# Kernel tuning notes

Hardware: AMD Instinct MI355X
Metric: run time of the kernel (lower is better)

The kernel has to match this reference:

```python
import jax, jax.numpy as jnp
from jax import lax
import numpy as np

# ---- static config (matches init_kwargs) ----
B, H, W = 8, 32, 32
L = H * W                      # 1024 tokens
D_MODEL = 384
MAMBA_DIM = 192                # d_model * d_mamba_ratio
LOCAL_DIM = 192
D_INNER = 384                  # expand_m * MAMBA_DIM
D_STATE = 16
D_CONV = 4
DT_RANK = 12                   # ceil(MAMBA_DIM / 16)
NDIR = 4                       # h, h_flip, v, v_flip
RED = 48                       # int(D_INNER * 0.125), BiAttn reduce dim
INNER_C = 192                  # LOCAL_DIM * expand_c
K_C = 8                        # local block depthwise kernel size


def setup_inputs() -> dict:
    key = jax.random.key(0)
    ks = jax.random.split(key, 16)
    s = 0.02
    return {
        "x": jax.random.normal(ks[0], (B, L, D_MODEL), jnp.float32),
        "in_proj_w": jax.random.normal(ks[1], (2 * D_INNER, MAMBA_DIM)) * s,
        "A_log": jnp.broadcast_to(jnp.log(jnp.arange(1, D_STATE + 1, dtype=jnp.float32)), (NDIR, D_INNER, D_STATE)) + 0.0,
        "conv_w": jax.random.normal(ks[2], (NDIR, D_INNER, D_CONV)) * 0.2,
        "conv_b": jax.random.normal(ks[3], (NDIR, D_INNER)) * 0.02,
        "xproj_w": jax.random.normal(ks[4], (NDIR, DT_RANK + 2 * D_STATE, D_INNER)) * s,
        "dtproj_w": jax.random.normal(ks[5], (NDIR, D_INNER, DT_RANK)) * (DT_RANK ** -0.5),
        "dtproj_b": jax.random.normal(ks[6], (NDIR, D_INNER)) * 0.5 - 4.0,
        "Dp": jnp.ones((NDIR, D_INNER)),
        "out_proj_w": jax.random.normal(ks[7], (MAMBA_DIM, D_INNER)) * s,
        "attn_ln_g": jnp.ones((D_INNER,)),
        "attn_ln_b": jnp.zeros((D_INNER,)),
        "attn_gr_w": jax.random.normal(ks[8], (RED, D_INNER)) * s,
        "attn_gr_b": jnp.zeros((RED,)),
        "attn_cs_w": jax.random.normal(ks[9], (D_INNER, RED)) * s,
        "attn_cs_b": jnp.zeros((D_INNER,)),
        "pw1_w": jax.random.normal(ks[10], (2 * INNER_C, LOCAL_DIM)) * s,
        "pw1_b": jnp.zeros((2 * INNER_C,)),
        "dw_w": jax.random.normal(ks[11], (INNER_C, K_C)) * 0.2,
        "dw_b": jnp.zeros((INNER_C,)),
        "bn_g": jnp.ones((INNER_C,)),
        "bn_b": jnp.zeros((INNER_C,)),
        "pw2_w": jax.random.normal(ks[12], (LOCAL_DIM, INNER_C)) * s,
        "pw2_b": jnp.zeros((LOCAL_DIM,)),
    }


def _forward(x, in_proj_w, A_log, conv_w, conv_b, xproj_w, dtproj_w, dtproj_b, Dp,
             out_proj_w, attn_ln_g, attn_ln_b, attn_gr_w, attn_gr_b, attn_cs_w, attn_cs_b,
             pw1_w, pw1_b, dw_w, dw_b, bn_g, bn_b, pw2_w, pw2_b):
    mamba_in = x[:, :, :MAMBA_DIM]
    local_in = x[:, :, MAMBA_DIM:]

    # ---------- MultiMamba branch ----------
    xz = jnp.swapaxes(mamba_in @ in_proj_w.T, 1, 2)   # (B, 2*D_INNER, L)

    def to_dir(t, i):
        # reorder channel-last-token axis per scan direction
        if i == 0:
            return t
        if i == 1:
            return jnp.flip(t, -1)
        tv = t.reshape(B, -1, H, W).swapaxes(-1, -2).reshape(B, -1, L)  # column-major scan
        return tv if i == 2 else jnp.flip(tv, -1)

    def from_dir(t, i):
        if i == 0:
            return t
        if i == 1:
            return jnp.flip(t, -1)
        if i == 3:
            t = jnp.flip(t, -1)
        return t.reshape(B, -1, W, H).swapaxes(-1, -2).reshape(B, -1, L)

    def ssm_dir(xzd, i):
        # mamba_inner_fn_no_out_proj: causal dwconv -> silu -> x_proj -> selective scan -> gate
        xp, z = jnp.split(xzd, 2, axis=1)            # (B, D_INNER, L) each
        xpad = jnp.pad(xp, ((0, 0), (0, 0), (D_CONV - 1, 0)))
        u = lax.conv_general_dilated(xpad, conv_w[i][:, None, :], (1,), 'VALID',
                                     dimension_numbers=('NCH', 'OIH', 'NCH'),
                                     feature_group_count=D_INNER)
        u = jax.nn.silu(u + conv_b[i][None, :, None])
        dbl = jnp.einsum('bdl,rd->brl', u, xproj_w[i])
        dt = dbl[:, :DT_RANK]
        Bm = dbl[:, DT_RANK:DT_RANK + D_STATE]
        Cm = dbl[:, DT_RANK + D_STATE:]
        delta = jax.nn.softplus(jnp.einsum('brl,dr->bdl', dt, dtproj_w[i]) + dtproj_b[i][None, :, None])
        A = -jnp.exp(A_log[i])                        # (D_INNER, D_STATE)

        def step(h, inps):
            d_t, B_t, C_t, u_t = inps                 # (B,d),(B,n),(B,n),(B,d)
            h = jnp.exp(d_t[:, :, None] * A) * h + (d_t * u_t)[:, :, None] * B_t[:, None, :]
            return h, jnp.einsum('bdn,bn->bd', h, C_t)

        h0 = jnp.zeros((B, D_INNER, D_STATE), x.dtype)
        _, ys = lax.scan(step, h0, (delta.transpose(2, 0, 1), Bm.transpose(2, 0, 1),
                                    Cm.transpose(2, 0, 1), u.transpose(2, 0, 1)))
        y = ys.transpose(1, 2, 0) + u * Dp[i][:, None]  # (B, D_INNER, L)
        return y * jax.nn.silu(z)

    def biattn(t):                                     # (B, L, D_INNER)
        mu = t.mean(-1, keepdims=True)
        var = ((t - mu) ** 2).mean(-1, keepdims=True)
        tn = (t - mu) / jnp.sqrt(var + 1e-5) * attn_ln_g + attn_ln_b
        g = tn.mean(1, keepdims=True)                  # global pool (B,1,D_INNER)
        g = jax.nn.gelu(g @ attn_gr_w.T + attn_gr_b, approximate=False)
        c = jax.nn.sigmoid(g @ attn_cs_w.T + attn_cs_b)
        return t * c

    acc = jnp.zeros((B, L, D_INNER), x.dtype)
    for i in range(NDIR):                              # fixed small set of directions
        out_i = from_dir(ssm_dir(to_dir(xz, i), i), i)
        acc = acc + biattn(jnp.swapaxes(out_i, 1, 2))
    mamba_out = acc @ out_proj_w.T                     # (B, L, MAMBA_DIM)

    # ---------- Local conv branch ----------
    hch = jnp.einsum('blc,oc->bol', local_in, pw1_w) + pw1_b[None, :, None]
    a, gte = jnp.split(hch, 2, axis=1)
    hch = a * jax.nn.sigmoid(gte)                      # GLU, (B, INNER_C, L)
    pad_l = K_C // 2
    pad_r = K_C // 2 - (K_C + 1) % 2                   # calc_same_padding(8) -> (4, 3)
    hpad = jnp.pad(hch, ((0, 0), (0, 0), (pad_l, pad_r)))
    hch = lax.conv_general_dilated(hpad, dw_w[:, None, :], (1,), 'VALID',
                                   dimension_numbers=('NCH', 'OIH', 'NCH'),
                                   feature_group_count=INNER_C) + dw_b[None, :, None]
    mu = hch.mean((0, 2))                              # BatchNorm1d (training-mode batch stats)
    var = hch.var((0, 2))
    hch = (hch - mu[None, :, None]) / jnp.sqrt(var + 1e-5)[None, :, None] * bn_g[None, :, None] + bn_b[None, :, None]
    hch = hch * jax.nn.sigmoid(hch)                    # Swish
    local_out = jnp.einsum('bcl,oc->blo', hch, pw2_w) + pw2_b

    return jnp.concatenate([mamba_out, local_out], axis=-1)


def reference(x, in_proj_w, A_log, conv_w, conv_b, xproj_w, dtproj_w, dtproj_b, Dp,
              out_proj_w, attn_ln_g, attn_ln_b, attn_gr_w, attn_gr_b, attn_cs_w, attn_cs_b,
              pw1_w, pw1_b, dw_w, dw_b, bn_g, bn_b, pw2_w, pw2_b):
    return _forward(x, in_proj_w, A_log, conv_w, conv_b, xproj_w, dtproj_w, dtproj_b, Dp,
                    out_proj_w, attn_ln_g, attn_ln_b, attn_gr_w, attn_gr_b, attn_cs_w, attn_cs_b,
                    pw1_w, pw1_b, dw_w, dw_b, bn_g, bn_b, pw2_w, pw2_b)
```

## Files before the change

kernel.cpp:

```cpp
#include <hip/hip_runtime.h>
#include <stdint.h>


#define DEV __device__ __forceinline__

typedef __attribute__((ext_vector_type(8))) short short8;
typedef __attribute__((ext_vector_type(4))) short short4v;
typedef __attribute__((ext_vector_type(4))) float f32x4;

DEV float bf(ushort v) { union { uint32_t u; float f; } c; c.u = ((uint32_t)v) << 16; return c.f; }
DEV ushort fbf(float f) {
  union { float f; uint32_t u; } c; c.f = f;
  uint32_t u = c.u;
  return (ushort)((u + 0x7FFFu + ((u >> 16) & 1u)) >> 16);
}

#if __has_builtin(__builtin_amdgcn_exp2f)
DEV float fexp2(float x) { return __builtin_amdgcn_exp2f(x); }
#else
DEV float fexp2(float x) { return __expf(x * 0.6931471805599453f); }
#endif

template<int CTRL>
DEV float rradd(float x) {
  return x + __int_as_float(__builtin_amdgcn_update_dpp(
      0, __float_as_int(x), CTRL, 0xF, 0xF, true));
}

DEV int pmap(int i, int j) {
  if (i == 0) return j;
  if (i == 1) return 1023 - j;
  if (i == 2) return ((j & 31) << 5) | (j >> 5);
  int k = 1023 - j; return ((k & 31) << 5) | (k >> 5);
}

DEV void cvt4(const float* __restrict__ s, ushort* __restrict__ d, int blk, int tid) {
  const int idx = (blk * 256 + tid) * 4;
  float4 v = *(const float4*)(s + idx);
  d[idx] = fbf(v.x); d[idx + 1] = fbf(v.y); d[idx + 2] = fbf(v.z); d[idx + 3] = fbf(v.w);
}

__global__ __launch_bounds__(256) void prep_all(
    const float* __restrict__ x, ushort* __restrict__ xb,
    const float* __restrict__ ipw, ushort* __restrict__ ipwb,
    const float* __restrict__ opw, ushort* __restrict__ opwb,
    const float* __restrict__ pw1w, ushort* __restrict__ pw1wb,
    const float* __restrict__ pw2w, ushort* __restrict__ pw2wb,
    const float* __restrict__ xw, ushort* __restrict__ xwp)
{
  const int bx = blockIdx.x, tid = threadIdx.x;
  if (bx < 3072)      cvt4(x, xb, bx, tid);
  else if (bx < 3216) cvt4(ipw, ipwb, bx - 3072, tid);
  else if (bx < 3288) cvt4(opw, opwb, bx - 3216, tid);
  else if (bx < 3360) cvt4(pw1w, pw1wb, bx - 3288, tid);
  else if (bx < 3396) cvt4(pw2w, pw2wb, bx - 3360, tid);
  else {
    const int row = bx - 3396;
    const int i = row >> 6, nn = row & 63;
    for (int c = tid; c < 384; c += 256)
      xwp[(size_t)row * 384 + c] = (nn < 44) ? fbf(xw[((size_t)i * 44 + nn) * 384 + c]) : (ushort)0;
  }
}

template<bool BF16OUT, bool BIAS>
__global__ __launch_bounds__(256) void gemm_bt(
    const ushort* __restrict__ A, long long sAz, int lda,
    const ushort* __restrict__ Bw, long long sBz,
    const float* __restrict__ bias,
    void* __restrict__ C, long long sCz, int ldc, int coff, int K)
{
  __shared__ ushort As[64][40];
  __shared__ ushort Bs[64][40];
  A += (size_t)blockIdx.z * sAz;
  Bw += (size_t)blockIdx.z * sBz;
  const int tid = threadIdx.x;
  const int m0 = blockIdx.x * 64, n0 = blockIdx.y * 64;
  const int w = tid >> 6, lane = tid & 63, l15 = lane & 15, quad = lane >> 4;
  const int sr = tid >> 2, sc = (tid & 3) * 8;
  f32x4 acc[4] = {};
  for (int k0 = 0; k0 < K; k0 += 32) {
    __syncthreads();
    *(short8*)&As[sr][sc] = *(const short8*)(A + (size_t)(m0 + sr) * lda + k0 + sc);
    *(short8*)&Bs[sr][sc] = *(const short8*)(Bw + (size_t)(n0 + sr) * K + k0 + sc);
    __syncthreads();
    short8 av = *(short8*)&As[w * 16 + l15][quad * 8];
#pragma unroll
    for (int nt = 0; nt < 4; nt++) {
      short8 bv = *(short8*)&Bs[nt * 16 + l15][quad * 8];
      acc[nt] = __builtin_amdgcn_mfma_f32_16x16x32_bf16(av, bv, acc[nt], 0, 0, 0);
    }
  }
  float* cf = (float*)C + (size_t)blockIdx.z * sCz;
  ushort* cb = (ushort*)C + (size_t)blockIdx.z * sCz;
#pragma unroll
  for (int nt = 0; nt < 4; nt++) {
    const int col = n0 + nt * 16 + l15;
    const float bv = BIAS ? bias[col] : 0.f;
#pragma unroll
    for (int r = 0; r < 4; r++) {
      const int row = m0 + w * 16 + quad * 4 + r;
      float v = acc[nt][r] + bv;
      if (BF16OUT) cb[(size_t)row * ldc + coff + col] = fbf(v);
      else         cf[(size_t)row * ldc + coff + col] = v;
    }
  }
}

__global__ __launch_bounds__(256) void gemm_dual(
    const ushort* __restrict__ A0, int lda0, const ushort* __restrict__ B0,
    const float* __restrict__ bias0, void* __restrict__ C0, int ldc0, int coff0, int K0,
    int nt0, int bf0,
    const ushort* __restrict__ A1, int lda1, const ushort* __restrict__ B1,
    const float* __restrict__ bias1, void* __restrict__ C1, int ldc1, int coff1, int K1,
    int bf1, float* __restrict__ bnsum)
{
  __shared__ ushort As[64][40];
  __shared__ ushort Bs[64][40];
  if (blockIdx.x == 0 && blockIdx.y == 0) {
    for (int k = threadIdx.x; k < 384; k += 256) bnsum[k] = 0.f;
  }
  const ushort* A; const ushort* Bw; const float* bias; void* C;
  int lda, ldc, coff, K, bf16o, n0;
  if ((int)blockIdx.y < nt0) {
    A = A0; lda = lda0; Bw = B0; bias = bias0; C = C0; ldc = ldc0; coff = coff0; K = K0;
    bf16o = bf0; n0 = blockIdx.y * 64;
  } else {
    A = A1; lda = lda1; Bw = B1; bias = bias1; C = C1; ldc = ldc1; coff = coff1; K = K1;
    bf16o = bf1; n0 = (blockIdx.y - nt0) * 64;
  }
  const int tid = threadIdx.x;
  const int m0 = blockIdx.x * 64;
  const int w = tid >> 6, lane = tid & 63, l15 = lane & 15, quad = lane >> 4;
  const int sr = tid >> 2, sc = (tid & 3) * 8;
  f32x4 acc[4] = {};
  for (int k0 = 0; k0 < K; k0 += 32) {
    __syncthreads();
    *(short8*)&As[sr][sc] = *(const short8*)(A + (size_t)(m0 + sr) * lda + k0 + sc);
    *(short8*)&Bs[sr][sc] = *(const short8*)(Bw + (size_t)(n0 + sr) * K + k0 + sc);
    __syncthreads();
    short8 av = *(short8*)&As[w * 16 + l15][quad * 8];
#pragma unroll
    for (int nt = 0; nt < 4; nt++) {
      short8 bv = *(short8*)&Bs[nt * 16 + l15][quad * 8];
      acc[nt] = __builtin_amdgcn_mfma_f32_16x16x32_bf16(av, bv, acc[nt], 0, 0, 0);
    }
  }
#pragma unroll
  for (int nt = 0; nt < 4; nt++) {
    const int col = n0 + nt * 16 + l15;
    const float bv = bias ? bias[col] : 0.f;
#pragma unroll
    for (int r = 0; r < 4; r++) {
      const int row = m0 + w * 16 + quad * 4 + r;
      float v = acc[nt][r] + bv;
      if (bf16o) ((ushort*)C)[(size_t)row * ldc + coff + col] = fbf(v);
      else       ((float*)C)[(size_t)row * ldc + coff + col] = v;
    }
  }
}

__global__ __launch_bounds__(256) void gemm_pw2(
    const float* __restrict__ h2, const float* __restrict__ bnsum,
    const float* __restrict__ bng, const float* __restrict__ bnb,
    const ushort* __restrict__ Bw, const float* __restrict__ bias,
    float* __restrict__ C)
{
  __shared__ ushort As[64][40];
  __shared__ ushort Bs[64][40];
  __shared__ float bsc[192], bsh[192];
  const int tid = threadIdx.x;
  const int m0 = blockIdx.x * 64, n0 = blockIdx.y * 64;
  const int w = tid >> 6, lane = tid & 63, l15 = lane & 15, quad = lane >> 4;
  const int sr = tid >> 2, sc = (tid & 3) * 8;
  for (int cth = tid; cth < 192; cth += 256) {
    float m = bnsum[cth] * (1.f / 8192.f);
    float va = bnsum[192 + cth] * (1.f / 8192.f) - m * m;
    float s = bng[cth] * rsqrtf(va + 1e-5f);
    bsc[cth] = s; bsh[cth] = bnb[cth] - m * s;
  }
  f32x4 acc[4] = {};
  for (int k0 = 0; k0 < 192; k0 += 32) {
    __syncthreads();
    {
      const float* hr = h2 + (size_t)(m0 + sr) * 192 + k0 + sc;
      f32x4 a0 = *(const f32x4*)(hr);
      f32x4 a1 = *(const f32x4*)(hr + 4);
      short8 v;
#pragma unroll
      for (int k = 0; k < 8; k++) {
        const float xx = (k < 4) ? a0[k] : a1[k - 4];
        const float xn = xx * bsc[k0 + sc + k] + bsh[k0 + sc + k];
        v[k] = (short)fbf(xn / (1.f + __expf(-xn)));
      }
      *(short8*)&As[sr][sc] = v;
    }
    *(short8*)&Bs[sr][sc] = *(const short8*)(Bw + (size_t)(n0 + sr) * 192 + k0 + sc);
    __syncthreads();
    short8 av = *(short8*)&As[w * 16 + l15][quad * 8];
#pragma unroll
    for (int nt = 0; nt < 4; nt++) {
      short8 bv = *(short8*)&Bs[nt * 16 + l15][quad * 8];
      acc[nt] = __builtin_amdgcn_mfma_f32_16x16x32_bf16(av, bv, acc[nt], 0, 0, 0);
    }
  }
#pragma unroll
  for (int nt = 0; nt < 4; nt++) {
    const int col = n0 + nt * 16 + l15;
    const float bv = bias[col];
#pragma unroll
    for (int r = 0; r < 4; r++) {
      const int row = m0 + w * 16 + quad * 4 + r;
      C[(size_t)row * 384 + 192 + col] = acc[nt][r] + bv;
    }
  }
}

__global__ __launch_bounds__(256) void convdbl_kernel(
    const ushort* __restrict__ xzb, const float* __restrict__ cw,
    const float* __restrict__ cb, const ushort* __restrict__ xwp,
    ushort* __restrict__ u, float* __restrict__ dbl)
{
  __shared__ __align__(16) ushort sxz[67][392];
  __shared__ float swt[384][4];
  __shared__ float scb[384];
  const int tid = threadIdx.x;
  const int i = blockIdx.y;
  const int m0 = blockIdx.x * 64;
  const int b = m0 >> 10, j0 = m0 & 1023;

  for (int k = tid; k < 1536; k += 256) ((float*)swt)[k] = cw[(size_t)i * 1536 + k];
  for (int k = tid; k < 384; k += 256) scb[k] = cb[i * 384 + k];
  for (int g = tid; g < 67 * 96; g += 256) {
    const int rr = g / 96, c4 = (g % 96) * 4;
    const int jj = j0 - 3 + rr;
    short4v v = {};
    if (jj >= 0)
      v = *(const short4v*)(xzb + (size_t)((b << 10) + pmap(i, jj)) * 768 + c4);
    *(short4v*)&sxz[rr][c4] = v;
  }
  __syncthreads();
  {
    const int r = tid >> 2, cp = tid & 3;
    ushort* ur = u + ((size_t)((i * 8 + b) << 10) + j0 + r) * 384 + cp * 96;
#pragma unroll 4
    for (int q = 0; q < 24; q++) {
      const int c = cp * 96 + q * 4;
      const short4v x0 = *(const short4v*)&sxz[r + 0][c];
      const short4v x1 = *(const short4v*)&sxz[r + 1][c];
      const short4v x2 = *(const short4v*)&sxz[r + 2][c];
      const short4v x3 = *(const short4v*)&sxz[r + 3][c];
      short4v o;
#pragma unroll
      for (int j = 0; j < 4; j++) {
        const f32x4 wv = *(const f32x4*)&swt[c + j][0];
        float s = bf((ushort)x0[j]) * wv[0] + bf((ushort)x1[j]) * wv[1]
                + bf((ushort)x2[j]) * wv[2] + bf((ushort)x3[j]) * wv[3] + scb[c + j];
        o[j] = (short)fbf(s / (1.f + __expf(-s)));
      }
      *(short4v*)(ur + q * 4) = o;
    }
  }
  ushort (*As)[40] = (ushort(*)[40])&sxz[0][0];
  ushort (*Bs)[40] = (ushort(*)[40])(&sxz[0][0] + 2560);
  const ushort* Au = u + (size_t)i * 8192 * 384;
  const ushort* Bw = xwp + (size_t)i * 64 * 384;
  const int w = tid >> 6, lane = tid & 63, l15 = lane & 15, quad = lane >> 4;
  const int sr = tid >> 2, sc = (tid & 3) * 8;
  f32x4 acc[4] = {};
  for (int k0 = 0; k0 < 384; k0 += 32) {
    __syncthreads();
    *(short8*)&As[sr][sc] = *(const short8*)(Au + (size_t)(m0 + sr) * 384 + k0 + sc);
    *(short8*)&Bs[sr][sc] = *(const short8*)(Bw + (size_t)sr * 384 + k0 + sc);
    __syncthreads();
    short8 av = *(short8*)&As[w * 16 + l15][quad * 8];
#pragma unroll
    for (int nt = 0; nt < 4; nt++) {
      short8 bv = *(short8*)&Bs[nt * 16 + l15][quad * 8];
      acc[nt] = __builtin_amdgcn_mfma_f32_16x16x32_bf16(av, bv, acc[nt], 0, 0, 0);
    }
  }
  float* cf = dbl + (size_t)i * 8192 * 64;
#pragma unroll
  for (int nt = 0; nt < 4; nt++) {
    const int col = nt * 16 + l15;
#pragma unroll
    for (int r = 0; r < 4; r++) {
      const int row = m0 + w * 16 + quad * 4 + r;
      cf[(size_t)row * 64 + col] = acc[nt][r];
    }
  }
}

#define NCH 16
#define CJ 64
__global__ __launch_bounds__(256, 3) void scan9b_kernel(
    const ushort* __restrict__ u,
    const float*  __restrict__ dbl,
    const ushort* __restrict__ xzb,
    const float* __restrict__ alog, const float* __restrict__ dtw,
    const float* __restrict__ dtb, const float* __restrict__ Dpw,
    ushort* __restrict__ y)
{
  const int dt0 = blockIdx.x * NCH;
  const int b = blockIdx.y, i = blockIdx.z;
  const int tid = threadIdx.x;
  const int ch = tid >> 4, n = tid & 15;
  const int srow = tid >> 2, role = tid & 3;

  __shared__ float sbc[2][CJ / 2][68];
  __shared__ float sdu[2][CJ / 2][68];
  __shared__ float sy[2][CJ][20];
  __shared__ float sDp[NCH];

  float w48[4][12], dtbv4[4];
#pragma unroll
  for (int cc = 0; cc < 4; cc++) {
    const int chp = 4 * role + cc;
#pragma unroll
    for (int r = 0; r < 12; r++) w48[cc][r] = dtw[((size_t)i * 384 + dt0 + chp) * 12 + r];
    dtbv4[cc] = dtb[i * 384 + dt0 + chp];
  }
  const float L2E = 1.4426950408889634f;
  const float Al = -__expf(alog[((size_t)i * 384 + dt0 + ch) * 16 + n]) * L2E;
  if (tid < NCH) sDp[tid] = Dpw[i * 384 + dt0 + tid];

  const float selm[4] = { (n >> 2) == 0 ? 1.f : 0.f, (n >> 2) == 1 ? 1.f : 0.f,
                          (n >> 2) == 2 ? 1.f : 0.f, (n >> 2) == 3 ? 1.f : 0.f };

  const size_t rb = (size_t)(i * 8 + b) << 10;
  const ushort* ub = u + rb * 384 + dt0;
  const float* dblb = dbl + rb * 64;
  const ushort* zb = xzb + ((size_t)b << 10) * 768 + 384 + dt0;
  ushort* yb = y + rb * 384 + dt0;

  f32x4 nd0, nd1, nd2, ns0, ns1, ns2; short4v nu, nz;
  {
    const float* src = dblb + (size_t)srow * 64;
    nd0 = *(const f32x4*)(src); nd1 = *(const f32x4*)(src + 4); nd2 = *(const f32x4*)(src + 8);
    const float* seg = src + role * 12;
    ns0 = *(const f32x4*)(seg); ns1 = *(const f32x4*)(seg + 4); ns2 = *(const f32x4*)(seg + 8);
    nu = *(const short4v*)(ub + (size_t)srow * 384 + 4 * role);
    nz = *(const short4v*)(zb + (size_t)pmap(i, srow) * 768 + 4 * role);
  }

  float h = 0.f;
  f32x4 ufp = {}, zfp = {};

  for (int c = 0; c < 16; c++) {
    const int bsel = c & 1;
    f32x4 uf, zf;
#pragma unroll
    for (int k = 0; k < 4; k++) { uf[k] = bf((ushort)nu[k]); zf[k] = bf((ushort)nz[k]); }
    if (role != 0) {
      float vals[12];
#pragma unroll
      for (int k = 0; k < 4; k++) { vals[k] = ns0[k]; vals[4 + k] = ns1[k]; vals[8 + k] = ns2[k]; }
#pragma unroll
      for (int k = 0; k < 12; k++) {
        const int f = role * 12 + k;
        if (f < 44) {
          const int isC = (f >= 28) ? 1 : 0;
          const int nn = isC ? (f - 28) : (f - 12);
          sbc[bsel][srow >> 1][4 * nn + 2 * (srow & 1) + isC] = vals[k];
        }
      }
    }
    {
      float dtr[12];
#pragma unroll
      for (int k = 0; k < 4; k++) { dtr[k] = nd0[k]; dtr[4 + k] = nd1[k]; dtr[8 + k] = nd2[k]; }
#pragma unroll
      for (int cc = 0; cc < 4; cc++) {
        float s = dtbv4[cc];
#pragma unroll
        for (int r = 0; r < 12; r++) s += dtr[r] * w48[cc][r];
        const float dl = fmaxf(s, 0.f) + __logf(1.f + __expf(-fabsf(s)));
        float2 pr; pr.x = dl; pr.y = dl * uf[cc];
        *(float2*)&sdu[bsel][srow >> 1][4 * (4 * role + cc) + 2 * (srow & 1)] = pr;
      }
    }
    __syncthreads();
    if (c > 0) {
      const int lo = pmap(i, (c - 1) * CJ + srow);
      const f32x4 y4 = *(const f32x4*)&sy[bsel ^ 1][srow][role * 4];
      short4v o;
#pragma unroll
      for (int t = 0; t < 4; t++) {
        const float z = zfp[t];
        const float val = (y4[t] + ufp[t] * sDp[role * 4 + t]) * (z / (1.f + __expf(-z)));
        o[t] = (short)fbf(val);
      }
      *(short4v*)(yb + (size_t)lo * 384 + role * 4) = o;
    }
    {
      const int cn = (c < 15) ? (c + 1) : 0;
      const int rown = cn * CJ + srow;
      const float* src = dblb + (size_t)rown * 64;
      nd0 = *(const f32x4*)(src); nd1 = *(const f32x4*)(src + 4); nd2 = *(const f32x4*)(src + 8);
      const float* seg = src + role * 12;
      ns0 = *(const f32x4*)(seg); ns1 = *(const f32x4*)(seg + 4); ns2 = *(const f32x4*)(seg + 8);
      nu = *(const short4v*)(ub + (size_t)rown * 384 + 4 * role);
      nz = *(const short4v*)(zb + (size_t)pmap(i, rown) * 768 + 4 * role);
    }
    const float* sduc = &sdu[bsel][0][4 * ch];
    const float* sbcc = &sbc[bsel][0][4 * n];
#pragma unroll
    for (int q = 0; q < 4; q++) {
      f32x4 pq = {0.f, 0.f, 0.f, 0.f};
#pragma unroll
      for (int s2 = 0; s2 < 8; s2++) {
        const f32x4 duP = *(const f32x4*)(sduc + (q * 8 + s2) * 68);
        const f32x4 bcP = *(const f32x4*)(sbcc + (q * 8 + s2) * 68);
        {
          const float e = fexp2(duP[0] * Al);
          h = e * h + duP[1] * bcP[0];
          float p = h * bcP[1];
          p = rradd<0x124>(p); p = rradd<0x128>(p);
          pq[s2 >> 1] = fmaf(selm[(2 * s2) & 3], p, pq[s2 >> 1]);
        }
        {
          const float e = fexp2(duP[2] * Al);
          h = e * h + duP[3] * bcP[2];
          float p = h * bcP[3];
          p = rradd<0x124>(p); p = rradd<0x128>(p);
          pq[s2 >> 1] = fmaf(selm[(2 * s2 + 1) & 3], p, pq[s2 >> 1]);
        }
      }
#pragma unroll
      for (int j = 0; j < 4; j++) {
        float t2 = rradd<0xB1>(pq[j]);
        t2 = rradd<0x4E>(t2);
        if ((n & 3) == 0) sy[bsel][(q << 4) | (j << 2) | (n >> 2)][ch] = t2;
      }
    }
    ufp = uf; zfp = zf;
  }
  __syncthreads();
  {
    const int lo = pmap(i, 15 * CJ + srow);
    const f32x4 y4 = *(const f32x4*)&sy[1][srow][role * 4];
    short4v o;
#pragma unroll
    for (int t = 0; t < 4; t++) {
      const float z = zfp[t];
      const float val = (y4[t] + ufp[t] * sDp[role * 4 + t]) * (z / (1.f + __expf(-z)));
      o[t] = (short)fbf(val);
    }
    *(short4v*)(yb + (size_t)lo * 384 + role * 4) = o;
  }
}

__global__ __launch_bounds__(256) void lngm_kernel(const ushort* __restrict__ y,
                                                   float* __restrict__ G16)
{
  const int slab = blockIdx.x, b = blockIdx.y, i = blockIdx.z;
  const int tid = threadIdx.x;
  const int w = tid >> 6, lane = tid & 63;
  __shared__ float smu[64], srs[64];
  __shared__ ushort sy16[64][384];
  const size_t base = (size_t)i * 8192 + b * 1024 + slab * 64;
  for (int rr = 0; rr < 16; rr++) {
    const int r = w * 16 + rr;
    const ushort* yr = y + (base + r) * 384;
    const short4v v4 = *(const short4v*)(yr + 4 * lane);
    const uint32_t v2 = *(const uint32_t*)(yr + 256 + 2 * lane);
    *(short4v*)&sy16[r][4 * lane] = v4;
    *(uint32_t*)&sy16[r][256 + 2 * lane] = v2;
    float s = 0.f, ss = 0.f;
#pragma unroll
    for (int t = 0; t < 4; t++) { float v = bf((ushort)v4[t]); s += v; ss += v * v; }
    { float v = bf((ushort)(v2 & 0xffffu)); s += v; ss += v * v; }
    { float v = bf((ushort)(v2 >> 16));     s += v; ss += v * v; }
#pragma unroll
    for (int off = 1; off < 64; off <<= 1) { s += __shfl_xor(s, off, 64); ss += __shfl_xor(ss, off, 64); }
    if (lane == 0) {
      float m = s * (1.f / 384.f);
      float va = ss * (1.f / 384.f) - m * m;
      smu[r] = m;
      srs[r] = rsqrtf(va + 1e-5f);
    }
  }
  __syncthreads();
  if (tid < 192) {
    const int c0 = tid * 2;
    float s0 = 0.f, s1 = 0.f;
#pragma unroll 8
    for (int r = 0; r < 64; r++) {
      const uint32_t pv = *(const uint32_t*)&sy16[r][c0];
      const float rs = srs[r], mu = smu[r];
      s0 += (bf((ushort)(pv & 0xffffu)) - mu) * rs;
      s1 += (bf((ushort)(pv >> 16)) - mu) * rs;
    }
    float* g = G16 + ((size_t)(i * 8 + b) * 16 + slab) * 384 + c0;
    g[0] = s0; g[1] = s1;
  }
}

__global__ __launch_bounds__(64) void gate_kernel(const float* __restrict__ G16,
    const float* __restrict__ lng, const float* __restrict__ lnb,
    const float* __restrict__ grw, const float* __restrict__ grb,
    const float* __restrict__ csw, const float* __restrict__ csb, float* __restrict__ cbuf)
{
  const int b = blockIdx.x, i = blockIdx.y;
  const int ib = i * 8 + b;
  const int lane = threadIdx.x;
  __shared__ float sG[384];
  __shared__ float g48[48];
  for (int dd = lane; dd < 384; dd += 64) {
    const float* g = G16 + (size_t)ib * 16 * 384 + dd;
    float s = 0.f;
#pragma unroll
    for (int k = 0; k < 16; k++) s += g[k * 384];
    sG[dd] = s * (1.f / 1024.f) * lng[dd] + lnb[dd];
  }
  __syncthreads();
  if (lane < 48) {
    float s = grb[lane];
    for (int dd = 0; dd < 384; dd++) s += sG[dd] * grw[lane * 384 + dd];
    g48[lane] = 0.5f * s * (1.f + erff(s * 0.70710678118f));
  }
  __syncthreads();
  for (int dd = lane; dd < 384; dd += 64) {
    float s = csb[dd];
#pragma unroll
    for (int r = 0; r < 48; r++) s += g48[r] * csw[dd * 48 + r];
    cbuf[(size_t)ib * 384 + dd] = 1.f / (1.f + __expf(-s));
  }
}

__global__ __launch_bounds__(384) void accgate_kernel(const ushort* __restrict__ y,
    const float* __restrict__ cbuf, ushort* __restrict__ accb)
{
  const int t = threadIdx.x;
  const int row = blockIdx.x * 4 + (t / 96);
  const int cg = (t % 96) * 4;
  const int b = row >> 10;
  f32x4 s = {};
#pragma unroll
  for (int i = 0; i < 4; i++) {
    const short4v v = *(const short4v*)(y + ((size_t)i * 8192 + row) * 384 + cg);
    const f32x4 cv = *(const f32x4*)(cbuf + (size_t)(i * 8 + b) * 384 + cg);
#pragma unroll
    for (int k = 0; k < 4; k++) s[k] += bf((ushort)v[k]) * cv[k];
  }
  short4v o;
#pragma unroll
  for (int k = 0; k < 4; k++) o[k] = (short)fbf(s[k]);
  *(short4v*)(accb + (size_t)row * 384 + cg) = o;
}

__global__ __launch_bounds__(192) void gludwbn_kernel(const ushort* __restrict__ hchb,
    const float* __restrict__ dww, const float* __restrict__ dwb,
    float* __restrict__ h2, float* __restrict__ bnsum)
{
  const int c = threadIdx.x;
  const int lt = blockIdx.x, b = blockIdx.y;
  __shared__ float sv[23][192];
  const int l0 = lt * 16;
#pragma unroll 4
  for (int r = 0; r < 23; r++) {
    const int ls = l0 + r - 4;
    float v = 0.f;
    if (ls >= 0 && ls < 1024) {
      const size_t rr = (size_t)((b << 10) + ls) * 384;
      const float a = bf(hchb[rr + c]);
      const float g = bf(hchb[rr + 192 + c]);
      v = a / (1.f + __expf(-g));
    }
    sv[r][c] = v;
  }
  __syncthreads();
  float wk[8];
#pragma unroll
  for (int k = 0; k < 8; k++) wk[k] = dww[(c << 3) + k];
  const float bias = dwb[c];
  float sacc = 0.f, ssacc = 0.f;
  for (int q = 0; q < 16; q++) {
    float s = bias;
#pragma unroll
    for (int k = 0; k < 8; k++) s += sv[q + k][c] * wk[k];
    h2[(size_t)((b << 10) + l0 + q) * 192 + c] = s;
    sacc += s; ssacc += s * s;
  }
  atomicAdd(&bnsum[c], sacc);
  atomicAdd(&bnsum[192 + c], ssacc);
}

extern "C" void kernel_launch(void* const* d_in, const int* in_sizes, int n_in,
                              void* d_out, int out_size, void* d_ws, size_t ws_size,
                              hipStream_t stream) {
  const float* x    = (const float*)d_in[0];
  const float* ipw  = (const float*)d_in[1];
  const float* alog = (const float*)d_in[2];
  const float* cw   = (const float*)d_in[3];
  const float* cbv  = (const float*)d_in[4];
  const float* xw   = (const float*)d_in[5];
  const float* dtw  = (const float*)d_in[6];
  const float* dtb  = (const float*)d_in[7];
  const float* Dpw  = (const float*)d_in[8];
  const float* opw  = (const float*)d_in[9];
  const float* lng  = (const float*)d_in[10];
  const float* lnb  = (const float*)d_in[11];
  const float* grw  = (const float*)d_in[12];
  const float* grb  = (const float*)d_in[13];
  const float* csw  = (const float*)d_in[14];
  const float* csb  = (const float*)d_in[15];
  const float* pw1w = (const float*)d_in[16];
  const float* pw1b = (const float*)d_in[17];
  const float* dww  = (const float*)d_in[18];
  const float* dwb  = (const float*)d_in[19];
  const float* bng  = (const float*)d_in[20];
  const float* bnb  = (const float*)d_in[21];
  const float* pw2w = (const float*)d_in[22];
  const float* pw2b = (const float*)d_in[23];
  float* out = (float*)d_out;

  char* ws = (char*)d_ws;
  ushort* xb    = (ushort*)(ws + 0);
  ushort* xzb   = (ushort*)(ws + 6291456);
  ushort* u     = (ushort*)(ws + 18874368);
  float*  dbl   = (float*)(ws + 44040192);
  ushort* y     = (ushort*)(ws + 52428800);
  ushort* accb  = (ushort*)(ws + 77594624);
  float*  G16   = (float*)(ws + 83886080);
  float*  cbuf  = (float*)(ws + 84672512);
  ushort* xwp   = (ushort*)(ws + 84721664);
  ushort* ipwb  = (ushort*)(ws + 84918272);
  ushort* opwb  = (ushort*)(ws + 85213184);
  ushort* pw1wb = (ushort*)(ws + 85360640);
  ushort* pw2wb = (ushort*)(ws + 85508096);
  float*  bnsum = (float*)(ws + 85581824);
  ushort* hchb = (ushort*)(ws + 18874368);
  float*  h2   = (float*)(ws + 34603008);

  prep_all<<<dim3(3652), 256, 0, stream>>>(x, xb, ipw, ipwb, opw, opwb,
                                           pw1w, pw1wb, pw2w, pw2wb, xw, xwp);
  gemm_bt<true, false><<<dim3(128, 12, 1), 256, 0, stream>>>(
      xb, 0, 384, ipwb, 0, nullptr, xzb, 0, 768, 0, 192);
  convdbl_kernel<<<dim3(128, 4), 256, 0, stream>>>(xzb, cw, cbv, xwp, u, dbl);
  scan9b_kernel<<<dim3(24, 8, 4), 256, 0, stream>>>(u, dbl, xzb, alog, dtw, dtb, Dpw, y);
  lngm_kernel<<<dim3(16, 8, 4), 256, 0, stream>>>(y, G16);
  gate_kernel<<<dim3(8, 4), 64, 0, stream>>>(G16, lng, lnb, grw, grb, csw, csb, cbuf);
  accgate_kernel<<<dim3(2048), 384, 0, stream>>>(y, cbuf, accb);
  gemm_dual<<<dim3(128, 9), 256, 0, stream>>>(
      accb, 384, opwb, nullptr, out, 384, 0, 384, 3, 0,
      xb + 192, 384, pw1wb, pw1b, hchb, 384, 0, 192, 1, bnsum);
  gludwbn_kernel<<<dim3(64, 8), 192, 0, stream>>>(hchb, dww, dwb, h2, bnsum);
  gemm_pw2<<<dim3(128, 3), 256, 0, stream>>>(h2, bnsum, bng, bnb, pw2wb, pw2b, out);
}
```

Baseline: 322.3 us.

## Pack scan delta and B/C operands as bf16 pairs in single-buffered LDS

The selective-scan kernel now stores dt and dt*u as two packed bf16 values per 32-bit word, and B and C the same way, instead of fp32 pairs. It also replaces the double-buffered shared arrays with a single buffer and writes each chunk's gated output inside the same iteration, after an extra barrier. This roughly halves LDS traffic per scan step and cuts shared-memory footprint, which may allow more resident blocks. In exchange the scan inputs lose precision, and the added per-chunk barrier removes the overlap between the output epilogue and the next chunk's staging.

```diff
diff --git a/kernel.cpp b/kernel.cpp
--- a/kernel.cpp
+++ b/kernel.cpp
@@ -7,8 +7,10 @@
 typedef __attribute__((ext_vector_type(8))) short short8;
 typedef __attribute__((ext_vector_type(4))) short short4v;
 typedef __attribute__((ext_vector_type(4))) float f32x4;
+typedef __attribute__((ext_vector_type(4))) uint32_t u32x4;
 
 DEV float bf(ushort v) { union { uint32_t u; float f; } c; c.u = ((uint32_t)v) << 16; return c.f; }
+DEV float fhi(uint32_t v) { union { uint32_t u; float f; } c; c.u = v; return c.f; }
 DEV ushort fbf(float f) {
   union { float f; uint32_t u; } c; c.f = f;
   uint32_t u = c.u;
@@ -293,7 +295,7 @@
 
 #define NCH 16
 #define CJ 64
-__global__ __launch_bounds__(256, 3) void scan9b_kernel(
+__global__ __launch_bounds__(256, 3) void scan11_kernel(
     const ushort* __restrict__ u,
     const float*  __restrict__ dbl,
     const ushort* __restrict__ xzb,
@@ -307,9 +309,9 @@
   const int ch = tid >> 4, n = tid & 15;
   const int srow = tid >> 2, role = tid & 3;
 
-  __shared__ float sbc[2][CJ / 2][68];
-  __shared__ float sdu[2][CJ / 2][68];
-  __shared__ float sy[2][CJ][20];
+  __shared__ __align__(16) uint32_t sduU[16 * 68];
+  __shared__ __align__(16) ushort   sbcU[16 * 136];
+  __shared__ float sy[CJ][20];
   __shared__ float sDp[NCH];
 
   float w48[4][12], dtbv4[4];
@@ -332,6 +334,8 @@
   const float* dblb = dbl + rb * 64;
   const ushort* zb = xzb + ((size_t)b << 10) * 768 + 384 + dt0;
   ushort* yb = y + rb * 384 + dt0;
+  const uint32_t* sdup = sduU + 4 * ch;
+  const uint32_t* sbcp = (const uint32_t*)sbcU + 4 * n;
 
   f32x4 nd0, nd1, nd2, ns0, ns1, ns2; short4v nu, nz;
   {
@@ -344,10 +348,9 @@
   }
 
   float h = 0.f;
-  f32x4 ufp = {}, zfp = {};
 
   for (int c = 0; c < 16; c++) {
-    const int bsel = c & 1;
+    const int j0 = c * CJ;
     f32x4 uf, zf;
 #pragma unroll
     for (int k = 0; k < 4; k++) { uf[k] = bf((ushort)nu[k]); zf[k] = bf((ushort)nz[k]); }
@@ -361,7 +364,7 @@
         if (f < 44) {
           const int isC = (f >= 28) ? 1 : 0;
           const int nn = isC ? (f - 28) : (f - 12);
-          sbc[bsel][srow >> 1][4 * nn + 2 * (srow & 1) + isC] = vals[k];
+          sbcU[(srow >> 2) * 136 + 8 * nn + 2 * (srow & 3) + isC] = fbf(vals[k]);
         }
       }
     }
@@ -375,23 +378,11 @@
 #pragma unroll
         for (int r = 0; r < 12; r++) s += dtr[r] * w48[cc][r];
         const float dl = fmaxf(s, 0.f) + __logf(1.f + __expf(-fabsf(s)));
-        float2 pr; pr.x = dl; pr.y = dl * uf[cc];
-        *(float2*)&sdu[bsel][srow >> 1][4 * (4 * role + cc) + 2 * (srow & 1)] = pr;
+        sduU[(srow >> 2) * 68 + (4 * role + cc) * 4 + (srow & 3)] =
+            ((uint32_t)fbf(dl * uf[cc]) << 16) | (uint32_t)fbf(dl);
       }
     }
     __syncthreads();
-    if (c > 0) {
-      const int lo = pmap(i, (c - 1) * CJ + srow);
-      const f32x4 y4 = *(const f32x4*)&sy[bsel ^ 1][srow][role * 4];
-      short4v o;
-#pragma unroll
-      for (int t = 0; t < 4; t++) {
-        const float z = zfp[t];
-        const float val = (y4[t] + ufp[t] * sDp[role * 4 + t]) * (z / (1.f + __expf(-z)));
-        o[t] = (short)fbf(val);
-      }
-      *(short4v*)(yb + (size_t)lo * 384 + role * 4) = o;
-    }
     {
       const int cn = (c < 15) ? (c + 1) : 0;
       const int rown = cn * CJ + srow;
@@ -402,51 +393,46 @@
       nu = *(const short4v*)(ub + (size_t)rown * 384 + 4 * role);
       nz = *(const short4v*)(zb + (size_t)pmap(i, rown) * 768 + 4 * role);
     }
-    const float* sduc = &sdu[bsel][0][4 * ch];
-    const float* sbcc = &sbc[bsel][0][4 * n];
 #pragma unroll
     for (int q = 0; q < 4; q++) {
       f32x4 pq = {0.f, 0.f, 0.f, 0.f};
 #pragma unroll
-      for (int s2 = 0; s2 < 8; s2++) {
-        const f32x4 duP = *(const f32x4*)(sduc + (q * 8 + s2) * 68);
-        const f32x4 bcP = *(const f32x4*)(sbcc + (q * 8 + s2) * 68);
-        {
-          const float e = fexp2(duP[0] * Al);
-          h = e * h + duP[1] * bcP[0];
-          float p = h * bcP[1];
+      for (int g = 0; g < 4; g++) {
+        const u32x4 du4 = *(const u32x4*)(sdup + (q * 4 + g) * 68);
+        const u32x4 bc4 = *(const u32x4*)(sbcp + (q * 4 + g) * 68);
+#pragma unroll
+        for (int t = 0; t < 4; t++) {
+          const float dl  = fhi(du4[t] << 16);
+          const float dlu = fhi(du4[t] & 0xffff0000u);
+          const float Bv  = fhi(bc4[t] << 16);
+          const float Cv  = fhi(bc4[t] & 0xffff0000u);
+          const float e = fexp2(dl * Al);
+          h = e * h + dlu * Bv;
+          float p = h * Cv;
           p = rradd<0x124>(p); p = rradd<0x128>(p);
-          pq[s2 >> 1] = fmaf(selm[(2 * s2) & 3], p, pq[s2 >> 1]);
-        }
-        {
-          const float e = fexp2(duP[2] * Al);
-          h = e * h + duP[3] * bcP[2];
-          float p = h * bcP[3];
-          p = rradd<0x124>(p); p = rradd<0x128>(p);
-          pq[s2 >> 1] = fmaf(selm[(2 * s2 + 1) & 3], p, pq[s2 >> 1]);
+          pq[g] = fmaf(selm[t], p, pq[g]);
         }
       }
 #pragma unroll
       for (int j = 0; j < 4; j++) {
         float t2 = rradd<0xB1>(pq[j]);
         t2 = rradd<0x4E>(t2);
-        if ((n & 3) == 0) sy[bsel][(q << 4) | (j << 2) | (n >> 2)][ch] = t2;
+        if ((n & 3) == 0) sy[(q << 4) | (j << 2) | (n >> 2)][ch] = t2;
       }
     }
-    ufp = uf; zfp = zf;
-  }
-  __syncthreads();
-  {
-    const int lo = pmap(i, 15 * CJ + srow);
-    const f32x4 y4 = *(const f32x4*)&sy[1][srow][role * 4];
-    short4v o;
-#pragma unroll
-    for (int t = 0; t < 4; t++) {
-      const float z = zfp[t];
-      const float val = (y4[t] + ufp[t] * sDp[role * 4 + t]) * (z / (1.f + __expf(-z)));
-      o[t] = (short)fbf(val);
-    }
-    *(short4v*)(yb + (size_t)lo * 384 + role * 4) = o;
+    __syncthreads();
+    {
+      const int lo = pmap(i, j0 + srow);
+      const f32x4 y4 = *(const f32x4*)&sy[srow][role * 4];
+      short4v o;
+#pragma unroll
+      for (int t = 0; t < 4; t++) {
+        const float z = zf[t];
+        const float val = (y4[t] + uf[t] * sDp[role * 4 + t]) * (z / (1.f + __expf(-z)));
+        o[t] = (short)fbf(val);
+      }
+      *(short4v*)(yb + (size_t)lo * 384 + role * 4) = o;
+    }
   }
 }
 
@@ -638,7 +624,7 @@
   gemm_bt<true, false><<<dim3(128, 12, 1), 256, 0, stream>>>(
       xb, 0, 384, ipwb, 0, nullptr, xzb, 0, 768, 0, 192);
   convdbl_kernel<<<dim3(128, 4), 256, 0, stream>>>(xzb, cw, cbv, xwp, u, dbl);
-  scan9b_kernel<<<dim3(24, 8, 4), 256, 0, stream>>>(u, dbl, xzb, alog, dtw, dtb, Dpw, y);
+  scan11_kernel<<<dim3(24, 8, 4), 256, 0, stream>>>(u, dbl, xzb, alog, dtw, dtb, Dpw, y);
   lngm_kernel<<<dim3(16, 8, 4), 256, 0, stream>>>(y, G16);
   gate_kernel<<<dim3(8, 4), 64, 0, stream>>>(G16, lng, lnb, grw, grb, csw, csb, cbuf);
   accgate_kernel<<<dim3(2048), 384, 0, stream>>>(y, cbuf, accb);
```

Result: slower. 339.6 us (+5.4%).
